# Kernel tuning notes

Measured on AMD Instinct MI355X. Metric: run time of the kernel, lower is better.

## Reference

```python
import jax, jax.numpy as jnp
import numpy as np

N = 16384      # bs(2048) * n_agents(8)
D_IN = 256     # input_shape
H = 256        # rnn_hidden_dim
E = 256        # hypernet_embed
A = 32         # n_actions


def setup_inputs() -> dict:
    key = jax.random.key(0)
    ks = jax.random.split(key, 18)
    s = 0.05
    f32 = jnp.float32
    return {
        "x": jax.random.normal(ks[0], (N, D_IN), f32),
        "h": jax.random.normal(ks[1], (N, H), f32) * 0.1,
        "fc1_w": jax.random.normal(ks[2], (D_IN, H), f32) * s,
        "fc1_b": jnp.zeros((H,), f32),
        "gru_w_ih": jax.random.normal(ks[3], (H, 3 * H), f32) * s,
        "gru_b_ih": jnp.zeros((3 * H,), f32),
        "gru_w_hh": jax.random.normal(ks[4], (H, 3 * H), f32) * s,
        "gru_b_hh": jnp.zeros((3 * H,), f32),
        "hg_w1": jax.random.normal(ks[5], (H, E), f32) * s,
        "hg_b1": jnp.zeros((E,), f32),
        "hg_w2": jax.random.normal(ks[6], (E, E), f32) * s,
        "hg_b2": jnp.zeros((E,), f32),
        "hb_w": jax.random.normal(ks[7], (E, A), f32) * s,
        "hb_b": jnp.zeros((A,), f32),
        "hw_w": jax.random.normal(ks[8], (E, H * A), f32) * s,
        "hw_b": jnp.zeros((H * A,), f32),
    }


def _gru_cell(x, h, w_ih, b_ih, w_hh, b_hh):
    # torch.nn.GRUCell semantics (gate order: r, z, n)
    gi = x @ w_ih + b_ih            # [N, 3H]
    gh = h @ w_hh + b_hh            # [N, 3H]
    i_r, i_z, i_n = jnp.split(gi, 3, axis=-1)
    h_r, h_z, h_n = jnp.split(gh, 3, axis=-1)
    r = jax.nn.sigmoid(i_r + h_r)
    z = jax.nn.sigmoid(i_z + h_z)
    n = jnp.tanh(i_n + r * h_n)
    return (1.0 - z) * n + z * h


def reference(x, h, fc1_w, fc1_b, gru_w_ih, gru_b_ih, gru_w_hh, gru_b_hh,
              hg_w1, hg_b1, hg_w2, hg_b2, hb_w, hb_b, hw_w, hw_b):
    x1 = jax.nn.relu(x @ fc1_w + fc1_b)                       # [N, H]
    hn = _gru_cell(x1, h, gru_w_ih, gru_b_ih, gru_w_hh, gru_b_hh)  # [N, H]
    # hypernet latent
    g = jnp.tanh(jax.nn.relu(hn @ hg_w1 + hg_b1) @ hg_w2 + hg_b2)  # [N, E]
    b_dyn = g @ hb_w + hb_b                                    # [N, A]
    w_dyn = (g @ hw_w + hw_b).reshape(hn.shape[0], H, A)       # [N, H, A]
    q = jnp.einsum('nh,nha->na', hn, w_dyn) + b_dyn            # [N, A]
    return q
```

## Files before the change

kernel.cpp:

```cpp
#include <hip/hip_runtime.h>


typedef _Float16 half8 __attribute__((ext_vector_type(8)));
typedef _Float16 half4 __attribute__((ext_vector_type(4)));
typedef float f32x4 __attribute__((ext_vector_type(4)));

#define MFMA16(a, b, c) __builtin_amdgcn_mfma_f32_16x16x32_f16((a), (b), (c), 0, 0, 0)

constexpr int NROWS = 16384;

__device__ __forceinline__ float sigmoidf_(float x) { return 1.0f / (1.0f + __expf(-x)); }

__device__ __forceinline__ void glds16(const void* g, void* l) {
    __builtin_amdgcn_global_load_lds((const __attribute__((address_space(1))) void*)g,
                                     (__attribute__((address_space(3))) void*)l, 16, 0, 0);
}

__global__ void prep_kernel(const float* __restrict__ x, const float* __restrict__ h,
                            const float* __restrict__ fc1_w, const float* __restrict__ hgw1,
                            const float* __restrict__ hgw2, const float* __restrict__ hbw,
                            const float* __restrict__ hww, const float* __restrict__ gwih,
                            const float* __restrict__ gwhh, _Float16* __restrict__ x16,
                            _Float16* __restrict__ xh, _Float16* __restrict__ w1t,
                            _Float16* __restrict__ hg1t, _Float16* __restrict__ hg2t,
                            _Float16* __restrict__ hbt, _Float16* __restrict__ hwt,
                            _Float16* __restrict__ wgru2, float* __restrict__ q) {
    __shared__ float tile[32][33];
    int b = blockIdx.x, tid = threadIdx.x;
    if (b < 4096) {
        int i = (b * 256 + tid) * 4;
        float4 v = *reinterpret_cast<const float4*>(x + i);
        x16[i + 0] = (_Float16)v.x; x16[i + 1] = (_Float16)v.y;
        x16[i + 2] = (_Float16)v.z; x16[i + 3] = (_Float16)v.w;
        return;
    }
    if (b < 8192) {
        int i = ((b - 4096) * 256 + tid) * 4;
        float4 v = *reinterpret_cast<const float4*>(h + i);
        int n = i >> 8, j = i & 255;
        _Float16* o = xh + n * 512 + 256 + j;
        o[0] = (_Float16)v.x; o[1] = (_Float16)v.y;
        o[2] = (_Float16)v.z; o[3] = (_Float16)v.w;
        return;
    }
    if (b >= 10824) {
        int zb = b - 10824;
        float4 z = {0.f, 0.f, 0.f, 0.f};
        *reinterpret_cast<float4*>(q + (size_t)(zb * 256 + tid) * 4) = z;
        return;
    }
    int tx = tid & 31, ty = tid >> 5;
    if (b < 10440) {
        int bb = b - 8192;
        const float* src; _Float16* dst; int C, idx;
        if (bb < 64)       { src = fc1_w; dst = w1t; C = 256;  idx = bb; }
        else if (bb < 128) { src = hgw1; dst = hg1t; C = 256;  idx = bb - 64; }
        else if (bb < 192) { src = hgw2; dst = hg2t; C = 256;  idx = bb - 128; }
        else if (bb < 200) { src = hbw;  dst = hbt;  C = 32;   idx = bb - 192; }
        else               { src = hww;  dst = hwt;  C = 8192; idx = bb - 200; }
        int kb = (idx & 7) * 32, cb = (idx >> 3) * 32;
#pragma unroll
        for (int i = ty; i < 32; i += 8) tile[i][tx] = src[(kb + i) * C + cb + tx];
        __syncthreads();
#pragma unroll
        for (int i = ty; i < 32; i += 8) {
            int c = cb + i, k = kb + tx;
            dst[c * 256 + (k ^ ((c & 7) << 3))] = (_Float16)tile[tx][i];
        }
        return;
    }
    {
        int bb = b - 10440, job = bb >> 6, idx = bb & 63;
        int kb = (idx & 7) * 32, cb = (idx >> 3) * 32;
        const float* src = (job & 1) ? gwhh : gwih;
        int gsub = job >> 1;
        int coff = (gsub < 2) ? gsub * 256 : 512;
        int koff = (job & 1) * 256;
#pragma unroll
        for (int i = ty; i < 32; i += 8) tile[i][tx] = src[(kb + i) * 768 + coff + cb + tx];
        __syncthreads();
#pragma unroll
        for (int i = ty; i < 32; i += 8) {
            int c = cb + i;
            int row = (c >> 4) * 48 + gsub * 16 + (c & 15);
            int kk = kb + tx + koff;
            wgru2[row * 512 + (kk ^ ((row & 7) << 3))] = (_Float16)tile[tx][i];
        }
    }
}

template <int ACT>
__global__ __launch_bounds__(256, 2) void gemm_lds_kernel(
    const _Float16* __restrict__ Am, const _Float16* __restrict__ Wt,
    const float* __restrict__ bias, _Float16* __restrict__ out16, int ONC) {
    __shared__ _Float16 Bs[64 * 256];
    const int tid = threadIdx.x, wave = tid >> 6, lane = tid & 63;
    const int r = lane & 15, kg = lane >> 4;
    const int row0 = blockIdx.x * 256 + wave * 64;
    const int col0 = blockIdx.y * 64;
    const _Float16* src = Wt + col0 * 256;
#pragma unroll
    for (int it = 0; it < 8; ++it)
        glds16(src + it * 2048 + tid * 8, Bs + it * 2048 + tid * 8);
    asm volatile("s_waitcnt vmcnt(0)" ::: "memory");
    __syncthreads();

    f32x4 z = {0.f, 0.f, 0.f, 0.f};
    f32x4 acc[4][4];
#pragma unroll
    for (int t = 0; t < 4; t++)
#pragma unroll
        for (int j = 0; j < 4; j++) acc[t][j] = z;
    const int swz = (r & 7) << 4;
#pragma unroll
    for (int kb = 0; kb < 8; kb++) {
        half8 a[4], bm[4];
#pragma unroll
        for (int t = 0; t < 4; t++)
            a[t] = *reinterpret_cast<const half8*>(Am + (row0 + t * 16 + r) * 256 + kb * 32 + kg * 8);
#pragma unroll
        for (int j = 0; j < 4; j++)
            bm[j] = *reinterpret_cast<const half8*>(
                (const char*)Bs + (j * 16 + r) * 512 + ((kb * 64 + kg * 16) ^ swz));
#pragma unroll
        for (int t = 0; t < 4; t++)
#pragma unroll
            for (int j = 0; j < 4; j++) acc[t][j] = MFMA16(a[t], bm[j], acc[t][j]);
    }
#pragma unroll
    for (int j = 0; j < 4; j++) {
        int cc = col0 + j * 16 + r;
        float bv = bias[cc];
#pragma unroll
        for (int t = 0; t < 4; t++)
#pragma unroll
            for (int i = 0; i < 4; i++) {
                int rr = row0 + t * 16 + kg * 4 + i;
                float v = acc[t][j][i] + bv;
                if (ACT == 1) v = fmaxf(v, 0.0f);
                if (ACT == 2) v = tanhf(v);
                out16[rr * ONC + cc] = (_Float16)v;
            }
    }
}

__global__ __launch_bounds__(256, 2) void gru_kernel(
    const _Float16* __restrict__ xh, const float* __restrict__ hf,
    const _Float16* __restrict__ wgru2, const float* __restrict__ bih,
    const float* __restrict__ bhh, _Float16* __restrict__ hn16,
    _Float16* __restrict__ hnT16) {
    __shared__ _Float16 Bs[48 * 512];
    const int tid = threadIdx.x, wave = tid >> 6, lane = tid & 63;
    const int r = lane & 15, kg = lane >> 4;
    const int row0 = blockIdx.x * 256 + wave * 64;
    const int c0 = blockIdx.y * 16;
    const _Float16* src = wgru2 + (size_t)blockIdx.y * 48 * 512;
#pragma unroll
    for (int it = 0; it < 12; ++it)
        glds16(src + it * 2048 + tid * 8, Bs + it * 2048 + tid * 8);
    asm volatile("s_waitcnt vmcnt(0)" ::: "memory");
    __syncthreads();

    f32x4 z = {0.f, 0.f, 0.f, 0.f};
    f32x4 ar[4], az[4], ain[4], ahn[4];
#pragma unroll
    for (int t = 0; t < 4; t++) { ar[t] = z; az[t] = z; ain[t] = z; ahn[t] = z; }
    const int swz = (r & 7) << 4;
#pragma unroll
    for (int kb = 0; kb < 16; kb++) {
        half8 a[4];
#pragma unroll
        for (int t = 0; t < 4; t++)
            a[t] = *reinterpret_cast<const half8*>(xh + (row0 + t * 16 + r) * 512 + kb * 32 + kg * 8);
        const int c0b = (kb * 64 + kg * 16) ^ swz;
        half8 br = *reinterpret_cast<const half8*>((const char*)Bs + (r) * 1024 + c0b);
        half8 bz = *reinterpret_cast<const half8*>((const char*)Bs + (16 + r) * 1024 + c0b);
        half8 bn = *reinterpret_cast<const half8*>((const char*)Bs + (32 + r) * 1024 + c0b);
#pragma unroll
        for (int t = 0; t < 4; t++) {
            ar[t] = MFMA16(a[t], br, ar[t]);
            az[t] = MFMA16(a[t], bz, az[t]);
        }
        if (kb < 8) {
#pragma unroll
            for (int t = 0; t < 4; t++) ain[t] = MFMA16(a[t], bn, ain[t]);
        } else {
#pragma unroll
            for (int t = 0; t < 4; t++) ahn[t] = MFMA16(a[t], bn, ahn[t]);
        }
    }
    const int cc = c0 + r;
    float brz = bih[cc] + bhh[cc];
    float bzz = bih[256 + cc] + bhh[256 + cc];
    float bin = bih[512 + cc], bhn = bhh[512 + cc];
    _Float16 vs[4][4];
#pragma unroll
    for (int t = 0; t < 4; t++)
#pragma unroll
        for (int i = 0; i < 4; i++) {
            int rr = row0 + t * 16 + kg * 4 + i;
            float rg = sigmoidf_(ar[t][i] + brz);
            float zg = sigmoidf_(az[t][i] + bzz);
            float nn = tanhf(ain[t][i] + bin + rg * (ahn[t][i] + bhn));
            float v = (1.0f - zg) * nn + zg * hf[rr * 256 + cc];
            _Float16 v16 = (_Float16)v;
            hn16[rr * 256 + cc] = v16;
            vs[t][i] = v16;
        }
    __syncthreads();
    _Float16* tileb = Bs;
#pragma unroll
    for (int t = 0; t < 4; t++)
#pragma unroll
        for (int i = 0; i < 4; i++)
            tileb[r * 264 + wave * 64 + t * 16 + kg * 4 + i] = vs[t][i];
    __syncthreads();
    {
        int trow = tid >> 4, chunk = tid & 15;
        half8 v0 = *reinterpret_cast<const half8*>(tileb + trow * 264 + chunk * 16);
        half8 v1 = *reinterpret_cast<const half8*>(tileb + trow * 264 + chunk * 16 + 8);
        size_t dst = (size_t)(c0 + trow) * NROWS + blockIdx.x * 256 + chunk * 16;
        *reinterpret_cast<half8*>(hnT16 + dst) = v0;
        *reinterpret_cast<half8*>(hnT16 + dst + 8) = v1;
    }
}

__global__ __launch_bounds__(256)
__attribute__((amdgpu_waves_per_eu(2, 2))) void final_kernel(
    const _Float16* __restrict__ g16, const _Float16* __restrict__ hwt,
    const float* __restrict__ hwb, const _Float16* __restrict__ hbt,
    const float* __restrict__ hbb, const _Float16* __restrict__ hnT16,
    float* __restrict__ q) {
    __shared__ _Float16 Bs[4][8192];
    __shared__ float hwbs[1024];
    const int bid = blockIdx.x;
    const int by = bid & 7, bx = bid >> 3;
    const int tid = threadIdx.x, wave = tid >> 6, lane = tid & 63;
    const int r = lane & 15, kg = lane >> 4;
    const int row0 = bx * 256 + wave * 64;
    const int hbase = by * 32;
    const int swz = (r & 7) << 4;

#pragma unroll
    for (int it = 0; it < 4; ++it) {
        int e = it * 2048 + tid * 8;
        glds16(hwt + (size_t)hbase * 8192 + e, &Bs[0][0] + e);
    }
    glds16(hwb + hbase * 32 + tid * 4, hwbs + tid * 4);

    half8 ga[4][8];
#pragma unroll
    for (int t = 0; t < 4; t++)
#pragma unroll
        for (int kb = 0; kb < 8; kb++)
            ga[t][kb] = *reinterpret_cast<const half8*>(
                g16 + (row0 + t * 16 + r) * 256 + kb * 32 + kg * 8);

    f32x4 qa[4][2];
    if (by == 0) {
        half8 hb0, hb1;
#pragma unroll
        for (int kb = 0; kb < 8; kb++) { (void)kb; }
        float b0v = hbb[r], b1v = hbb[16 + r];
#pragma unroll
        for (int t = 0; t < 4; t++) {
            qa[t][0] = {b0v, b0v, b0v, b0v};
            qa[t][1] = {b1v, b1v, b1v, b1v};
        }
#pragma unroll
        for (int kb = 0; kb < 8; kb++) {
            const int c0b = (kb * 64 + kg * 16) ^ swz;
            hb0 = *reinterpret_cast<const half8*>((const char*)hbt + r * 512 + c0b);
            hb1 = *reinterpret_cast<const half8*>((const char*)hbt + (16 + r) * 512 + c0b);
#pragma unroll
            for (int t = 0; t < 4; t++) {
                qa[t][0] = MFMA16(ga[t][kb], hb0, qa[t][0]);
                qa[t][1] = MFMA16(ga[t][kb], hb1, qa[t][1]);
            }
        }
    } else {
        f32x4 z = {0.f, 0.f, 0.f, 0.f};
#pragma unroll
        for (int t = 0; t < 4; t++) { qa[t][0] = z; qa[t][1] = z; }
    }
#pragma unroll
    for (int t = 0; t < 4; t++)
#pragma unroll
        for (int kb = 0; kb < 8; kb++)
            asm volatile("" : "+v"(ga[t][kb]));

    asm volatile("s_waitcnt vmcnt(0)" ::: "memory");
    __builtin_amdgcn_s_barrier();

#pragma unroll
    for (int it = 0; it < 4; ++it) {
        int e = it * 2048 + tid * 8;
        glds16(hwt + (size_t)(hbase + 1) * 8192 + e, &Bs[1][0] + e);
    }
    const _Float16* hvbase = hnT16 + (size_t)hbase * NROWS + bx * 256 + wave * 64 + kg * 4;
    half4 hvA[4], hvB[4];
#pragma unroll
    for (int t = 0; t < 4; t++) hvA[t] = *reinterpret_cast<const half4*>(hvbase + t * 16);

    auto phase = [&](int h, half4* hvC, half4* hvN) {
        if (h < 30) {
            const _Float16* srcp = hwt + (size_t)(hbase + h + 2) * 8192;
            _Float16* dst = &Bs[(h + 2) & 3][0];
#pragma unroll
            for (int it = 0; it < 4; ++it) {
                int e = it * 2048 + tid * 8;
                glds16(srcp + e, dst + e);
            }
        }
        if (h < 31) {
            const _Float16* hp = hvbase + (size_t)(h + 1) * NROWS;
#pragma unroll
            for (int t = 0; t < 4; t++) hvN[t] = *reinterpret_cast<const half4*>(hp + t * 16);
        }
        if (h < 30)
            asm volatile("s_waitcnt vmcnt(8)" ::: "memory");
        else if (h == 30)
            asm volatile("s_waitcnt vmcnt(4)" ::: "memory");
        else
            asm volatile("s_waitcnt vmcnt(0)" ::: "memory");
        __builtin_amdgcn_s_barrier();

        const char* bp = (const char*)&Bs[h & 3][0];
        float wb0 = hwbs[(h << 5) + r], wb1 = hwbs[(h << 5) + 16 + r];
        f32x4 w0[4], w1[4];
#pragma unroll
        for (int t = 0; t < 4; t++) {
            w0[t] = {wb0, wb0, wb0, wb0};
            w1[t] = {wb1, wb1, wb1, wb1};
        }
        __builtin_amdgcn_s_setprio(1);
#pragma unroll
        for (int kb = 0; kb < 8; kb++) {
            const int c0b = (kb * 64 + kg * 16) ^ swz;
            half8 b0 = *reinterpret_cast<const half8*>(bp + r * 512 + c0b);
            half8 b1 = *reinterpret_cast<const half8*>(bp + (16 + r) * 512 + c0b);
#pragma unroll
            for (int t = 0; t < 4; t++) {
                w0[t] = MFMA16(ga[t][kb], b0, w0[t]);
                w1[t] = MFMA16(ga[t][kb], b1, w1[t]);
            }
        }
        __builtin_amdgcn_s_setprio(0);
#pragma unroll
        for (int t = 0; t < 4; t++)
#pragma unroll
            for (int i = 0; i < 4; i++) {
                float hvf = (float)hvC[t][i];
                qa[t][0][i] += hvf * w0[t][i];
                qa[t][1][i] += hvf * w1[t][i];
            }
    };
    for (int h = 0; h < 32; h += 2) {
        phase(h, hvA, hvB);
        phase(h + 1, hvB, hvA);
    }

#pragma unroll
    for (int t = 0; t < 4; t++)
#pragma unroll
        for (int i = 0; i < 4; i++) {
            int rr = row0 + t * 16 + kg * 4 + i;
            atomicAdd(&q[rr * 32 + r], qa[t][0][i]);
            atomicAdd(&q[rr * 32 + 16 + r], qa[t][1][i]);
        }
}

extern "C" void kernel_launch(void* const* d_in, const int* in_sizes, int n_in,
                              void* d_out, int out_size, void* d_ws, size_t ws_size,
                              hipStream_t stream) {
    const float* x = (const float*)d_in[0];
    const float* h = (const float*)d_in[1];
    const float* fc1_w = (const float*)d_in[2];
    const float* fc1_b = (const float*)d_in[3];
    const float* gwih = (const float*)d_in[4];
    const float* gbih = (const float*)d_in[5];
    const float* gwhh = (const float*)d_in[6];
    const float* gbhh = (const float*)d_in[7];
    const float* hgw1 = (const float*)d_in[8];
    const float* hgb1 = (const float*)d_in[9];
    const float* hgw2 = (const float*)d_in[10];
    const float* hgb2 = (const float*)d_in[11];
    const float* hbw = (const float*)d_in[12];
    const float* hbb = (const float*)d_in[13];
    const float* hww = (const float*)d_in[14];
    const float* hwb = (const float*)d_in[15];
    float* q = (float*)d_out;

    char* p = (char*)d_ws;
    auto alloc = [&](size_t bytes) { char* r = p; p += (bytes + 255) & ~255ULL; return r; };
    _Float16* x16 = (_Float16*)alloc((size_t)NROWS * 256 * 2);
    _Float16* xh = (_Float16*)alloc((size_t)NROWS * 512 * 2);
    _Float16* w1t = (_Float16*)alloc((size_t)256 * 256 * 2);
    _Float16* wgru2 = (_Float16*)alloc((size_t)768 * 512 * 2);
    _Float16* hg1t = (_Float16*)alloc((size_t)256 * 256 * 2);
    _Float16* hg2t = (_Float16*)alloc((size_t)256 * 256 * 2);
    _Float16* hbt = (_Float16*)alloc((size_t)32 * 256 * 2);
    _Float16* hwt = (_Float16*)alloc((size_t)8192 * 256 * 2 + 65536);
    _Float16* hn16 = (_Float16*)alloc((size_t)NROWS * 256 * 2);
    _Float16* hnT16 = (_Float16*)alloc((size_t)256 * NROWS * 2);
    _Float16* t16 = (_Float16*)alloc((size_t)NROWS * 256 * 2);
    _Float16* g16 = (_Float16*)alloc((size_t)NROWS * 256 * 2);

    prep_kernel<<<11336, 256, 0, stream>>>(x, h, fc1_w, hgw1, hgw2, hbw, hww, gwih, gwhh,
                                           x16, xh, w1t, hg1t, hg2t, hbt, hwt, wgru2, q);

    gemm_lds_kernel<1><<<dim3(64, 4), 256, 0, stream>>>(x16, w1t, fc1_b, xh, 512);

    gru_kernel<<<dim3(64, 16), 256, 0, stream>>>(xh, h, wgru2, gbih, gbhh, hn16, hnT16);

    gemm_lds_kernel<1><<<dim3(64, 4), 256, 0, stream>>>(hn16, hg1t, hgb1, t16, 256);
    gemm_lds_kernel<2><<<dim3(64, 4), 256, 0, stream>>>(t16, hg2t, hgb2, g16, 256);

    final_kernel<<<512, 256, 0, stream>>>(g16, hwt, hwb, hbt, hbb, hnT16, q);
}
```

Measured before the change: 159.5 us.

## Fold hidden-state scaling into MFMA A operand and drop transposed hn buffer

The final kernel now multiplies each row's g fragment by the broadcast hn value before the MFMA and accumulates straight into q. Previously it built the per-h dynamic weights in separate accumulators and applied hn with a scalar FMA epilogue. The hw bias term becomes its own small MFMA against a re-laid-out fp16 bias matrix, so the GRU kernel no longer writes a transposed hn copy through LDS. Weight layouts in prep are changed to a k-blocked form so B-fragment loads need no XOR swizzle. This trades epilogue FMAs and the transposed write for per-phase half8 multiplies, scalar strided hn loads, and extra fp16 rounding of the g*hn products.

```diff
diff --git a/kernel.cpp b/kernel.cpp
--- a/kernel.cpp
+++ b/kernel.cpp
@@ -2,7 +2,6 @@
 
 
 typedef _Float16 half8 __attribute__((ext_vector_type(8)));
-typedef _Float16 half4 __attribute__((ext_vector_type(4)));
 typedef float f32x4 __attribute__((ext_vector_type(4)));
 
 #define MFMA16(a, b, c) __builtin_amdgcn_mfma_f32_16x16x32_f16((a), (b), (c), 0, 0, 0)
@@ -20,11 +19,12 @@
                             const float* __restrict__ fc1_w, const float* __restrict__ hgw1,
                             const float* __restrict__ hgw2, const float* __restrict__ hbw,
                             const float* __restrict__ hww, const float* __restrict__ gwih,
-                            const float* __restrict__ gwhh, _Float16* __restrict__ x16,
-                            _Float16* __restrict__ xh, _Float16* __restrict__ w1t,
-                            _Float16* __restrict__ hg1t, _Float16* __restrict__ hg2t,
-                            _Float16* __restrict__ hbt, _Float16* __restrict__ hwt,
-                            _Float16* __restrict__ wgru2, float* __restrict__ q) {
+                            const float* __restrict__ gwhh, const float* __restrict__ hwb,
+                            _Float16* __restrict__ x16, _Float16* __restrict__ xh,
+                            _Float16* __restrict__ w1t, _Float16* __restrict__ hg1t,
+                            _Float16* __restrict__ hg2t, _Float16* __restrict__ hbt,
+                            _Float16* __restrict__ hwt, _Float16* __restrict__ wgru2,
+                            _Float16* __restrict__ hwb2, float* __restrict__ q) {
     __shared__ float tile[32][33];
     int b = blockIdx.x, tid = threadIdx.x;
     if (b < 4096) {
@@ -43,6 +43,17 @@
         o[2] = (_Float16)v.z; o[3] = (_Float16)v.w;
         return;
     }
+    if (b >= 11336) {
+        int i = ((b - 11336) * 256 + tid) * 4;
+        float4 v = *reinterpret_cast<const float4*>(hwb + i);
+        float arr[4] = {v.x, v.y, v.z, v.w};
+#pragma unroll
+        for (int j = 0; j < 4; j++) {
+            int e = i + j, hh = e >> 5, a = e & 31;
+            hwb2[(hh >> 3) * 256 + a * 8 + (hh & 7)] = (_Float16)arr[j];
+        }
+        return;
+    }
     if (b >= 10824) {
         int zb = b - 10824;
         float4 z = {0.f, 0.f, 0.f, 0.f};
@@ -52,12 +63,12 @@
     int tx = tid & 31, ty = tid >> 5;
     if (b < 10440) {
         int bb = b - 8192;
-        const float* src; _Float16* dst; int C, idx;
-        if (bb < 64)       { src = fc1_w; dst = w1t; C = 256;  idx = bb; }
-        else if (bb < 128) { src = hgw1; dst = hg1t; C = 256;  idx = bb - 64; }
-        else if (bb < 192) { src = hgw2; dst = hg2t; C = 256;  idx = bb - 128; }
-        else if (bb < 200) { src = hbw;  dst = hbt;  C = 32;   idx = bb - 192; }
-        else               { src = hww;  dst = hwt;  C = 8192; idx = bb - 200; }
+        const float* src; _Float16* dst; int C, idx, mode;
+        if (bb < 64)       { src = fc1_w; dst = w1t;  C = 256;  idx = bb;       mode = 0; }
+        else if (bb < 128) { src = hgw1;  dst = hg1t; C = 256;  idx = bb - 64;  mode = 0; }
+        else if (bb < 192) { src = hgw2;  dst = hg2t; C = 256;  idx = bb - 128; mode = 0; }
+        else if (bb < 200) { src = hbw;   dst = hbt;  C = 32;   idx = bb - 192; mode = 1; }
+        else               { src = hww;   dst = hwt;  C = 8192; idx = bb - 200; mode = 2; }
         int kb = (idx & 7) * 32, cb = (idx >> 3) * 32;
 #pragma unroll
         for (int i = ty; i < 32; i += 8) tile[i][tx] = src[(kb + i) * C + cb + tx];
@@ -65,7 +76,14 @@
 #pragma unroll
         for (int i = ty; i < 32; i += 8) {
             int c = cb + i, k = kb + tx;
-            dst[c * 256 + (k ^ ((c & 7) << 3))] = (_Float16)tile[tx][i];
+            if (mode == 0) {
+                dst[c * 256 + (k ^ ((c & 7) << 3))] = (_Float16)tile[tx][i];
+            } else if (mode == 1) {
+                dst[(k >> 3) * 256 + c * 8 + (k & 7)] = (_Float16)tile[tx][i];
+            } else {
+                int hh = c >> 5, a = c & 31;
+                dst[hh * 8192 + (k >> 3) * 256 + a * 8 + (k & 7)] = (_Float16)tile[tx][i];
+            }
         }
         return;
     }
@@ -147,8 +165,7 @@
 __global__ __launch_bounds__(256, 2) void gru_kernel(
     const _Float16* __restrict__ xh, const float* __restrict__ hf,
     const _Float16* __restrict__ wgru2, const float* __restrict__ bih,
-    const float* __restrict__ bhh, _Float16* __restrict__ hn16,
-    _Float16* __restrict__ hnT16) {
+    const float* __restrict__ bhh, _Float16* __restrict__ hn16) {
     __shared__ _Float16 Bs[48 * 512];
     const int tid = threadIdx.x, wave = tid >> 6, lane = tid & 63;
     const int r = lane & 15, kg = lane >> 4;
@@ -193,7 +210,6 @@
     float brz = bih[cc] + bhh[cc];
     float bzz = bih[256 + cc] + bhh[256 + cc];
     float bin = bih[512 + cc], bhn = bhh[512 + cc];
-    _Float16 vs[4][4];
 #pragma unroll
     for (int t = 0; t < 4; t++)
 #pragma unroll
@@ -203,50 +219,29 @@
             float zg = sigmoidf_(az[t][i] + bzz);
             float nn = tanhf(ain[t][i] + bin + rg * (ahn[t][i] + bhn));
             float v = (1.0f - zg) * nn + zg * hf[rr * 256 + cc];
-            _Float16 v16 = (_Float16)v;
-            hn16[rr * 256 + cc] = v16;
-            vs[t][i] = v16;
-        }
-    __syncthreads();
-    _Float16* tileb = Bs;
-#pragma unroll
-    for (int t = 0; t < 4; t++)
-#pragma unroll
-        for (int i = 0; i < 4; i++)
-            tileb[r * 264 + wave * 64 + t * 16 + kg * 4 + i] = vs[t][i];
-    __syncthreads();
-    {
-        int trow = tid >> 4, chunk = tid & 15;
-        half8 v0 = *reinterpret_cast<const half8*>(tileb + trow * 264 + chunk * 16);
-        half8 v1 = *reinterpret_cast<const half8*>(tileb + trow * 264 + chunk * 16 + 8);
-        size_t dst = (size_t)(c0 + trow) * NROWS + blockIdx.x * 256 + chunk * 16;
-        *reinterpret_cast<half8*>(hnT16 + dst) = v0;
-        *reinterpret_cast<half8*>(hnT16 + dst + 8) = v1;
-    }
+            hn16[rr * 256 + cc] = (_Float16)v;
+        }
 }
 
 __global__ __launch_bounds__(256)
 __attribute__((amdgpu_waves_per_eu(2, 2))) void final_kernel(
     const _Float16* __restrict__ g16, const _Float16* __restrict__ hwt,
-    const float* __restrict__ hwb, const _Float16* __restrict__ hbt,
-    const float* __restrict__ hbb, const _Float16* __restrict__ hnT16,
+    const _Float16* __restrict__ hwb2, const _Float16* __restrict__ hbt,
+    const float* __restrict__ hbb, const _Float16* __restrict__ hn16,
     float* __restrict__ q) {
     __shared__ _Float16 Bs[4][8192];
-    __shared__ float hwbs[1024];
     const int bid = blockIdx.x;
     const int by = bid & 7, bx = bid >> 3;
     const int tid = threadIdx.x, wave = tid >> 6, lane = tid & 63;
     const int r = lane & 15, kg = lane >> 4;
     const int row0 = bx * 256 + wave * 64;
     const int hbase = by * 32;
-    const int swz = (r & 7) << 4;
 
 #pragma unroll
     for (int it = 0; it < 4; ++it) {
         int e = it * 2048 + tid * 8;
         glds16(hwt + (size_t)hbase * 8192 + e, &Bs[0][0] + e);
     }
-    glds16(hwb + hbase * 32 + tid * 4, hwbs + tid * 4);
 
     half8 ga[4][8];
 #pragma unroll
@@ -258,9 +253,6 @@
 
     f32x4 qa[4][2];
     if (by == 0) {
-        half8 hb0, hb1;
-#pragma unroll
-        for (int kb = 0; kb < 8; kb++) { (void)kb; }
         float b0v = hbb[r], b1v = hbb[16 + r];
 #pragma unroll
         for (int t = 0; t < 4; t++) {
@@ -269,15 +261,31 @@
         }
 #pragma unroll
         for (int kb = 0; kb < 8; kb++) {
-            const int c0b = (kb * 64 + kg * 16) ^ swz;
-            hb0 = *reinterpret_cast<const half8*>((const char*)hbt + r * 512 + c0b);
-            hb1 = *reinterpret_cast<const half8*>((const char*)hbt + (16 + r) * 512 + c0b);
+            const char* hp = (const char*)hbt + (kb * 4 + kg) * 512 + r * 16;
+            half8 hb0 = *reinterpret_cast<const half8*>(hp);
+            half8 hb1 = *reinterpret_cast<const half8*>(hp + 256);
 #pragma unroll
             for (int t = 0; t < 4; t++) {
                 qa[t][0] = MFMA16(ga[t][kb], hb0, qa[t][0]);
                 qa[t][1] = MFMA16(ga[t][kb], hb1, qa[t][1]);
             }
         }
+#pragma unroll
+        for (int kb = 0; kb < 8; kb++) {
+            half8 an[4];
+#pragma unroll
+            for (int t = 0; t < 4; t++)
+                an[t] = *reinterpret_cast<const half8*>(
+                    hn16 + (row0 + t * 16 + r) * 256 + kb * 32 + kg * 8);
+            const char* wp = (const char*)hwb2 + (kb * 4 + kg) * 512 + r * 16;
+            half8 wb0 = *reinterpret_cast<const half8*>(wp);
+            half8 wb1 = *reinterpret_cast<const half8*>(wp + 256);
+#pragma unroll
+            for (int t = 0; t < 4; t++) {
+                qa[t][0] = MFMA16(an[t], wb0, qa[t][0]);
+                qa[t][1] = MFMA16(an[t], wb1, qa[t][1]);
+            }
+        }
     } else {
         f32x4 z = {0.f, 0.f, 0.f, 0.f};
 #pragma unroll
@@ -297,12 +305,12 @@
         int e = it * 2048 + tid * 8;
         glds16(hwt + (size_t)(hbase + 1) * 8192 + e, &Bs[1][0] + e);
     }
-    const _Float16* hvbase = hnT16 + (size_t)hbase * NROWS + bx * 256 + wave * 64 + kg * 4;
-    half4 hvA[4], hvB[4];
-#pragma unroll
-    for (int t = 0; t < 4; t++) hvA[t] = *reinterpret_cast<const half4*>(hvbase + t * 16);
-
-    auto phase = [&](int h, half4* hvC, half4* hvN) {
+    const _Float16* hnp = hn16 + (size_t)(row0 + r) * 256 + hbase;
+    _Float16 hnA[4], hnB[4];
+#pragma unroll
+    for (int t = 0; t < 4; t++) hnA[t] = hnp[t * 4096];
+
+    auto phase = [&](int h, _Float16* hnC, _Float16* hnN) {
         if (h < 30) {
             const _Float16* srcp = hwt + (size_t)(hbase + h + 2) * 8192;
             _Float16* dst = &Bs[(h + 2) & 3][0];
@@ -313,9 +321,8 @@
             }
         }
         if (h < 31) {
-            const _Float16* hp = hvbase + (size_t)(h + 1) * NROWS;
-#pragma unroll
-            for (int t = 0; t < 4; t++) hvN[t] = *reinterpret_cast<const half4*>(hp + t * 16);
+#pragma unroll
+            for (int t = 0; t < 4; t++) hnN[t] = hnp[t * 4096 + h + 1];
         }
         if (h < 30)
             asm volatile("s_waitcnt vmcnt(8)" ::: "memory");
@@ -326,38 +333,30 @@
         __builtin_amdgcn_s_barrier();
 
         const char* bp = (const char*)&Bs[h & 3][0];
-        float wb0 = hwbs[(h << 5) + r], wb1 = hwbs[(h << 5) + 16 + r];
-        f32x4 w0[4], w1[4];
+        half8 s[4];
 #pragma unroll
         for (int t = 0; t < 4; t++) {
-            w0[t] = {wb0, wb0, wb0, wb0};
-            w1[t] = {wb1, wb1, wb1, wb1};
+            _Float16 v = hnC[t];
+            s[t] = (half8){v, v, v, v, v, v, v, v};
         }
         __builtin_amdgcn_s_setprio(1);
 #pragma unroll
         for (int kb = 0; kb < 8; kb++) {
-            const int c0b = (kb * 64 + kg * 16) ^ swz;
-            half8 b0 = *reinterpret_cast<const half8*>(bp + r * 512 + c0b);
-            half8 b1 = *reinterpret_cast<const half8*>(bp + (16 + r) * 512 + c0b);
+            const char* kp = bp + (kb * 4 + kg) * 512 + r * 16;
+            half8 b0 = *reinterpret_cast<const half8*>(kp);
+            half8 b1 = *reinterpret_cast<const half8*>(kp + 256);
 #pragma unroll
             for (int t = 0; t < 4; t++) {
-                w0[t] = MFMA16(ga[t][kb], b0, w0[t]);
-                w1[t] = MFMA16(ga[t][kb], b1, w1[t]);
+                half8 ap = ga[t][kb] * s[t];
+                qa[t][0] = MFMA16(ap, b0, qa[t][0]);
+                qa[t][1] = MFMA16(ap, b1, qa[t][1]);
             }
         }
         __builtin_amdgcn_s_setprio(0);
-#pragma unroll
-        for (int t = 0; t < 4; t++)
-#pragma unroll
-            for (int i = 0; i < 4; i++) {
-                float hvf = (float)hvC[t][i];
-                qa[t][0][i] += hvf * w0[t][i];
-                qa[t][1][i] += hvf * w1[t][i];
-            }
     };
     for (int h = 0; h < 32; h += 2) {
-        phase(h, hvA, hvB);
-        phase(h + 1, hvB, hvA);
+        phase(h, hnA, hnB);
+        phase(h + 1, hnB, hnA);
     }
 
 #pragma unroll
@@ -401,20 +400,21 @@
     _Float16* hg2t = (_Float16*)alloc((size_t)256 * 256 * 2);
     _Float16* hbt = (_Float16*)alloc((size_t)32 * 256 * 2);
     _Float16* hwt = (_Float16*)alloc((size_t)8192 * 256 * 2 + 65536);
+    _Float16* hwb2 = (_Float16*)alloc((size_t)8192 * 2);
     _Float16* hn16 = (_Float16*)alloc((size_t)NROWS * 256 * 2);
-    _Float16* hnT16 = (_Float16*)alloc((size_t)256 * NROWS * 2);
     _Float16* t16 = (_Float16*)alloc((size_t)NROWS * 256 * 2);
     _Float16* g16 = (_Float16*)alloc((size_t)NROWS * 256 * 2);
 
-    prep_kernel<<<11336, 256, 0, stream>>>(x, h, fc1_w, hgw1, hgw2, hbw, hww, gwih, gwhh,
-                                           x16, xh, w1t, hg1t, hg2t, hbt, hwt, wgru2, q);
+    prep_kernel<<<11344, 256, 0, stream>>>(x, h, fc1_w, hgw1, hgw2, hbw, hww, gwih, gwhh,
+                                           hwb, x16, xh, w1t, hg1t, hg2t, hbt, hwt, wgru2,
+                                           hwb2, q);
 
     gemm_lds_kernel<1><<<dim3(64, 4), 256, 0, stream>>>(x16, w1t, fc1_b, xh, 512);
 
-    gru_kernel<<<dim3(64, 16), 256, 0, stream>>>(xh, h, wgru2, gbih, gbhh, hn16, hnT16);
+    gru_kernel<<<dim3(64, 16), 256, 0, stream>>>(xh, h, wgru2, gbih, gbhh, hn16);
 
     gemm_lds_kernel<1><<<dim3(64, 4), 256, 0, stream>>>(hn16, hg1t, hgb1, t16, 256);
     gemm_lds_kernel<2><<<dim3(64, 4), 256, 0, stream>>>(t16, hg2t, hgb2, g16, 256);
 
-    final_kernel<<<512, 256, 0, stream>>>(g16, hwt, hwb, hbt, hbb, hnT16, q);
-}
+    final_kernel<<<512, 256, 0, stream>>>(g16, hwt, hwb2, hbt, hbb, hn16, q);
+}
```

Result: slower. 173.5 us (+8.7%).
